# Kernel optimization log

Measured on AMD Instinct MI355X. Metric: run time of the kernel, lower is better.

Reference implementation:

```python
import jax, jax.numpy as jnp
import numpy as np

N = 100000
E = 1600000
NEG_SLOPE = 0.2


def gat_layer(x, W, al, ar, b, src, dst):
    """DGL GATConv (no dropout, no residual, bias=True, activation=None).
    x: [N, in]; W: [in, H*D]; al, ar, b: [H, D]. Returns [N, H, D]."""
    H, D = al.shape
    feat = (x @ W).reshape(N, H, D)               # [N,H,D]
    el = jnp.sum(feat * al, axis=-1)              # [N,H]
    er = jnp.sum(feat * ar, axis=-1)              # [N,H]
    e = jax.nn.leaky_relu(el[src] + er[dst], NEG_SLOPE)  # [E,H]
    # segment softmax over incoming edges of each dst node
    emax = jax.lax.stop_gradient(jax.ops.segment_max(e, dst, num_segments=N))
    ex = jnp.exp(e - emax[dst])                   # [E,H]
    denom = jax.ops.segment_sum(ex, dst, num_segments=N)  # [N,H]
    alpha = ex / jnp.where(denom[dst] == 0, 1.0, denom[dst])  # [E,H]
    msg = feat[src] * alpha[..., None]            # [E,H,D] gather + weight
    out = jax.ops.segment_sum(msg, dst, num_segments=N)    # [N,H,D] scatter-add
    return out + b[None, :, :]


def setup_inputs() -> dict:
    key = jax.random.key(0)
    ks = jax.random.split(key, 12)
    in_size, hid, out_size, heads = 128, 32, 16, 4
    x = jax.random.normal(ks[0], (N, in_size), dtype=jnp.float32)
    src = jax.random.randint(ks[1], (E,), 0, N, dtype=jnp.int32)
    dst = jax.random.randint(ks[2], (E,), 0, N, dtype=jnp.int32)
    W1 = jax.random.normal(ks[3], (in_size, heads * hid), dtype=jnp.float32) * (1.0 / np.sqrt(in_size))
    al1 = jax.random.normal(ks[4], (heads, hid), dtype=jnp.float32) * 0.1
    ar1 = jax.random.normal(ks[5], (heads, hid), dtype=jnp.float32) * 0.1
    b1 = jnp.zeros((heads, hid), dtype=jnp.float32)
    W2 = jax.random.normal(ks[6], (hid, out_size), dtype=jnp.float32) * (1.0 / np.sqrt(hid))
    al2 = jax.random.normal(ks[7], (1, out_size), dtype=jnp.float32) * 0.1
    ar2 = jax.random.normal(ks[8], (1, out_size), dtype=jnp.float32) * 0.1
    b2 = jnp.zeros((1, out_size), dtype=jnp.float32)
    return {"x": x, "src": src, "dst": dst, "W1": W1, "al1": al1, "ar1": ar1,
            "b1": b1, "W2": W2, "al2": al2, "ar2": ar2, "b2": b2}


def reference(x, src, dst, W1, al1, ar1, b1, W2, al2, ar2, b2):
    h = gat_layer(x, W1, al1, ar1, b1, src, dst)   # [N, heads, hid]
    h = jax.nn.relu(jnp.mean(h, axis=1))           # mean over heads + relu
    h = gat_layer(h, W2, al2, ar2, b2, src, dst)   # [N, 1, out]
    return h.reshape(N, -1)                        # flatten
```

## Files before the change

kernel.cpp:

```cpp
#include <hip/hip_runtime.h>
#include <hip/hip_bf16.h>

#define NEG_SLOPE 0.2f
#define LOG2E 1.44269504f
#define G_SHIFT 7
#define GSZ 128
#define CHUNK 4096

typedef __attribute__((ext_vector_type(8))) __bf16 bf16x8;
typedef __attribute__((ext_vector_type(4))) float f32x4;

__device__ __forceinline__ unsigned short f2bf(float f) {
    unsigned u = __float_as_uint(f);
    unsigned r = (u + 0x7fffu + ((u >> 16) & 1u)) >> 16;
    return (unsigned short)r;
}
__device__ __forceinline__ float bflo(unsigned v) { return __uint_as_float(v << 16); }
__device__ __forceinline__ float bfhi(unsigned v) { return __uint_as_float(v & 0xffff0000u); }

__global__ __launch_bounds__(256) void coarse_scatter(
    const int* __restrict__ src, const int* __restrict__ dst,
    int* __restrict__ gcursor, unsigned* __restrict__ inter, int NB, int E) {
    __shared__ int hist[800];
    __shared__ int lbase[800];
    __shared__ int gbase[800];
    __shared__ unsigned stage[CHUNK];
    __shared__ unsigned short bstage[CHUNK];

    const int tid = threadIdx.x;
    const int e0 = blockIdx.x * CHUNK;
    const int cnt = min(CHUNK, E - e0);

    for (int i = tid; i < NB; i += 256) hist[i] = 0;
    __syncthreads();

    unsigned pk[16];
    int bb[16];
#pragma unroll
    for (int r = 0; r < 16; ++r) {
        int idx = tid + r * 256;
        if (idx < cnt) {
            int s = src[e0 + idx];
            int d = dst[e0 + idx];
            pk[r] = ((unsigned)s << G_SHIFT) | (unsigned)(d & (GSZ - 1));
            bb[r] = d >> G_SHIFT;
            atomicAdd(&hist[bb[r]], 1);
        }
    }
    __syncthreads();
    if (tid < 64) {
        int carry = 0;
        for (int i = 0; i < NB; i += 64) {
            int v = (i + tid < NB) ? hist[i + tid] : 0;
            int xv = v;
            for (int o = 1; o < 64; o <<= 1) {
                int tt = __shfl_up(xv, o, 64);
                if (tid >= o) xv += tt;
            }
            if (i + tid < NB) lbase[i + tid] = carry + xv - v;
            carry += __shfl(xv, 63, 64);
        }
    }
    __syncthreads();
    for (int i = tid; i < NB; i += 256) {
        int hh = hist[i];
        gbase[i] = (hh > 0) ? (i * CHUNK + atomicAdd(&gcursor[i], hh)) : 0;
    }
    __syncthreads();
    for (int i = tid; i < NB; i += 256) hist[i] = 0;
    __syncthreads();
#pragma unroll
    for (int r = 0; r < 16; ++r) {
        int idx = tid + r * 256;
        if (idx < cnt) {
            int b = bb[r];
            int rk = atomicAdd(&hist[b], 1);
            int pos = lbase[b] + rk;
            stage[pos] = pk[r];
            bstage[pos] = (unsigned short)b;
        }
    }
    __syncthreads();
#pragma unroll
    for (int r = 0; r < 16; ++r) {
        int idx = tid + r * 256;
        if (idx < cnt) {
            int b = (int)bstage[idx];
            inter[gbase[b] + (idx - lbase[b])] = stage[idx];
        }
    }
}

__global__ __launch_bounds__(256) void fine_scatter(
    const unsigned* __restrict__ inter, const int* __restrict__ gcursor,
    int* __restrict__ deg, int* __restrict__ rowptr, int* __restrict__ esrc,
    int N, int NB) {
    __shared__ int h[GSZ];
    __shared__ int lb[GSZ];
    __shared__ int stage[CHUNK];
    __shared__ int redsum[256];
    const int b = blockIdx.x;
    const int tid = threadIdx.x;
    const int cnt = gcursor[b];
    const unsigned* ep = inter + (size_t)b * CHUNK;

    {
        int s = 0;
        for (int i = tid; i < b; i += 256) s += gcursor[i];
        redsum[tid] = s;
        __syncthreads();
        for (int o = 128; o > 0; o >>= 1) {
            if (tid < o) redsum[tid] += redsum[tid + o];
            __syncthreads();
        }
    }
    const int base = redsum[0];

    if (tid < GSZ) h[tid] = 0;
    __syncthreads();

    int ss[16];
    unsigned char ln[16];
    int nr = 0;
    for (int idx = tid; idx < cnt; idx += 256) {
        unsigned ed = ep[idx];
        ss[nr] = (int)(ed >> G_SHIFT);
        int l = (int)(ed & (GSZ - 1));
        ln[nr++] = (unsigned char)l;
        atomicAdd(&h[l], 1);
    }
    __syncthreads();
    if (tid < 64) {
        int carry = 0;
        for (int i = 0; i < GSZ; i += 64) {
            int v = h[i + tid];
            int xv = v;
            for (int o = 1; o < 64; o <<= 1) {
                int tt = __shfl_up(xv, o, 64);
                if (tid >= o) xv += tt;
            }
            lb[i + tid] = carry + xv - v;
            carry += __shfl(xv, 63, 64);
        }
    }
    __syncthreads();
    if (tid < GSZ) {
        int node = b * GSZ + tid;
        if (node < N) {
            deg[node] = h[tid];
            rowptr[node] = base + lb[tid];
        }
        h[tid] = 0;
    }
    __syncthreads();
    for (int r = 0; r < nr; ++r) {
        int l = ln[r];
        int rk = atomicAdd(&h[l], 1);
        stage[lb[l] + rk] = ss[r];
    }
    __syncthreads();
    for (int idx = tid; idx < cnt; idx += 256) esrc[base + idx] = stage[idx];
}

__global__ __launch_bounds__(128) void wconv_kernel(
    const float* __restrict__ W, unsigned short* __restrict__ wtb) {
    int c = blockIdx.x;
    int k = threadIdx.x;
    wtb[c * 128 + k] = f2bf(W[k * 128 + c]);
}

#define GSTRIDE 136
__global__ __launch_bounds__(256) void gemm1_mfma(
    const float* __restrict__ x, const unsigned short* __restrict__ wtb,
    const float* __restrict__ al, const float* __restrict__ ar,
    unsigned short* __restrict__ featb, float* __restrict__ el,
    float* __restrict__ er, int N) {
    __shared__ unsigned short xs[128][GSTRIDE];
    __shared__ unsigned short ws[128][GSTRIDE];
    const int t = threadIdx.x;
    const int m0 = blockIdx.x * 128;
    const int w = t >> 6;
    const int l = t & 63;
    const int lr = l & 15;
    const int lg = l >> 4;

    {
        const uint4* wv = (const uint4*)wtb;
#pragma unroll
        for (int rr = 0; rr < 8; ++rr) {
            int q = t + 256 * rr;
            int c = q >> 4, kb = q & 15;
            uint4 v = wv[q];
            *((uint4*)&ws[c][kb * 8]) = v;
        }
    }
    {
#pragma unroll
        for (int rr = 0; rr < 16; ++rr) {
            int q = t + 256 * rr;
            int row = q >> 5, c4 = q & 31;
            int gm = m0 + row;
            if (gm >= N) gm = N - 1;
            float4 v = *((const float4*)(x + (size_t)gm * 128 + c4 * 4));
            ushort4 o;
            o.x = f2bf(v.x); o.y = f2bf(v.y); o.z = f2bf(v.z); o.w = f2bf(v.w);
            *((ushort4*)&xs[row][c4 * 4]) = o;
        }
    }
    __syncthreads();

    f32x4 acc[2][8];
#pragma unroll
    for (int i = 0; i < 2; ++i)
#pragma unroll
        for (int j = 0; j < 8; ++j) acc[i][j] = (f32x4){0.f, 0.f, 0.f, 0.f};

#pragma unroll
    for (int kk = 0; kk < 4; ++kk) {
        const int k0 = kk * 32 + lg * 8;
        bf16x8 a0 = *((const bf16x8*)&xs[w * 32 + lr][k0]);
        bf16x8 a1 = *((const bf16x8*)&xs[w * 32 + 16 + lr][k0]);
#pragma unroll
        for (int nj = 0; nj < 8; ++nj) {
            bf16x8 bfr = *((const bf16x8*)&ws[nj * 16 + lr][k0]);
            acc[0][nj] = __builtin_amdgcn_mfma_f32_16x16x32_bf16(a0, bfr, acc[0][nj], 0, 0, 0);
            acc[1][nj] = __builtin_amdgcn_mfma_f32_16x16x32_bf16(a1, bfr, acc[1][nj], 0, 0, 0);
        }
    }
    __syncthreads();
#pragma unroll
    for (int mi = 0; mi < 2; ++mi)
#pragma unroll
        for (int r = 0; r < 4; ++r) {
            int row = w * 32 + mi * 16 + lg * 4 + r;
#pragma unroll
            for (int nj = 0; nj < 8; ++nj)
                xs[row][nj * 16 + lr] = f2bf(acc[mi][nj][r]);
        }
    __syncthreads();
    {
        int row = t >> 1, half = t & 1;
        int gm = m0 + row;
        if (gm < N) {
            float pl0 = 0.f, pl1 = 0.f, pr0 = 0.f, pr1 = 0.f;
            const unsigned short* xr = &xs[row][half * 64];
            uint4* outp = (uint4*)(featb + (size_t)gm * 128 + half * 64);
#pragma unroll
            for (int b8 = 0; b8 < 8; ++b8) {
                uint4 v = *((const uint4*)(xr + b8 * 8));
                int cb = half * 64 + b8 * 8;
                float4 a0 = *((const float4*)(al + cb));
                float4 a1 = *((const float4*)(al + cb + 4));
                float4 r0 = *((const float4*)(ar + cb));
                float4 r1 = *((const float4*)(ar + cb + 4));
                float f0 = bflo(v.x), f1 = bfhi(v.x), f2 = bflo(v.y), f3 = bfhi(v.y);
                float f4 = bflo(v.z), f5 = bfhi(v.z), f6 = bflo(v.w), f7 = bfhi(v.w);
                float sl = f0 * a0.x + f1 * a0.y + f2 * a0.z + f3 * a0.w
                         + f4 * a1.x + f5 * a1.y + f6 * a1.z + f7 * a1.w;
                float sr = f0 * r0.x + f1 * r0.y + f2 * r0.z + f3 * r0.w
                         + f4 * r1.x + f5 * r1.y + f6 * r1.z + f7 * r1.w;
                if (b8 < 4) { pl0 += sl; pr0 += sr; } else { pl1 += sl; pr1 += sr; }
                outp[b8] = v;
            }
            el[gm * 4 + half * 2 + 0] = pl0 * LOG2E;
            el[gm * 4 + half * 2 + 1] = pl1 * LOG2E;
            er[gm * 4 + half * 2 + 0] = pr0 * LOG2E;
            er[gm * 4 + half * 2 + 1] = pr1 * LOG2E;
        }
    }
}

__global__ __launch_bounds__(256) void pull1_kernel(
    const int* __restrict__ rowptr, const int* __restrict__ deg,
    const int* __restrict__ esrc, const float* __restrict__ el,
    const float* __restrict__ er, const unsigned short* __restrict__ featb,
    const float* __restrict__ b,
    const float* __restrict__ W2, const float* __restrict__ al2,
    const float* __restrict__ ar2, float* __restrict__ feat2,
    float* __restrict__ el2, float* __restrict__ er2, int N) {
    int tid = blockIdx.x * 256 + threadIdx.x;
    int node = tid >> 4;
    int lane = threadIdx.x & 15;
    if (node >= N) return;
    int h = lane >> 2;
    int dq = lane & 3;
    int start = rowptr[node];
    int cnt = deg[node];
    float er_nh = er[node * 4 + h];
    const int* ep = esrc + start;
    const unsigned short* fb = featb + h * 32 + dq * 8;

    float acc[8];
#pragma unroll
    for (int j = 0; j < 8; ++j) acc[j] = 0.f;
    float sumex = 0.f;

    int i = 0;
    for (; i + 8 <= cnt; i += 8) {
        int s[8]; float e[8]; uint4 u[8];
#pragma unroll
        for (int j = 0; j < 8; ++j) s[j] = ep[i + j];
#pragma unroll
        for (int j = 0; j < 8; ++j) u[j] = *((const uint4*)(fb + (size_t)s[j] * 128));
#pragma unroll
        for (int j = 0; j < 8; ++j) e[j] = el[s[j] * 4 + h];
#pragma unroll
        for (int j = 0; j < 8; ++j) {
            float v = e[j] + er_nh;
            v = fmaxf(v, NEG_SLOPE * v);
            float xx = exp2f(v);
            sumex += xx;
            acc[0] += xx * bflo(u[j].x); acc[1] += xx * bfhi(u[j].x);
            acc[2] += xx * bflo(u[j].y); acc[3] += xx * bfhi(u[j].y);
            acc[4] += xx * bflo(u[j].z); acc[5] += xx * bfhi(u[j].z);
            acc[6] += xx * bflo(u[j].w); acc[7] += xx * bfhi(u[j].w);
        }
    }
    for (; i + 4 <= cnt; i += 4) {
        int s[4]; float e[4]; uint4 u[4];
#pragma unroll
        for (int j = 0; j < 4; ++j) s[j] = ep[i + j];
#pragma unroll
        for (int j = 0; j < 4; ++j) u[j] = *((const uint4*)(fb + (size_t)s[j] * 128));
#pragma unroll
        for (int j = 0; j < 4; ++j) e[j] = el[s[j] * 4 + h];
#pragma unroll
        for (int j = 0; j < 4; ++j) {
            float v = e[j] + er_nh;
            v = fmaxf(v, NEG_SLOPE * v);
            float xx = exp2f(v);
            sumex += xx;
            acc[0] += xx * bflo(u[j].x); acc[1] += xx * bfhi(u[j].x);
            acc[2] += xx * bflo(u[j].y); acc[3] += xx * bfhi(u[j].y);
            acc[4] += xx * bflo(u[j].z); acc[5] += xx * bfhi(u[j].z);
            acc[6] += xx * bflo(u[j].w); acc[7] += xx * bfhi(u[j].w);
        }
    }
    for (; i < cnt; ++i) {
        int s = ep[i];
        float v = el[s * 4 + h] + er_nh;
        v = fmaxf(v, NEG_SLOPE * v);
        float xx = exp2f(v);
        sumex += xx;
        uint4 u = *((const uint4*)(fb + (size_t)s * 128));
        acc[0] += xx * bflo(u.x); acc[1] += xx * bfhi(u.x);
        acc[2] += xx * bflo(u.y); acc[3] += xx * bfhi(u.y);
        acc[4] += xx * bflo(u.z); acc[5] += xx * bfhi(u.z);
        acc[6] += xx * bflo(u.w); acc[7] += xx * bfhi(u.w);
    }

    float inv = 1.f / ((sumex == 0.f) ? 1.f : sumex);
    float4 bb0 = *((const float4*)(b + h * 32 + dq * 8));
    float4 bb1 = *((const float4*)(b + h * 32 + dq * 8 + 4));
    float o[8];
    o[0] = acc[0] * inv + bb0.x; o[1] = acc[1] * inv + bb0.y;
    o[2] = acc[2] * inv + bb0.z; o[3] = acc[3] * inv + bb0.w;
    o[4] = acc[4] * inv + bb1.x; o[5] = acc[5] * inv + bb1.y;
    o[6] = acc[6] * inv + bb1.z; o[7] = acc[7] * inv + bb1.w;
#pragma unroll
    for (int j = 0; j < 8; ++j) {
        o[j] += __shfl_xor(o[j], 4);
        o[j] += __shfl_xor(o[j], 8);
        o[j] = fmaxf(o[j] * 0.25f, 0.f);
    }
    int c = lane;
    float fc = 0.f;
#pragma unroll
    for (int q = 0; q < 4; ++q) {
#pragma unroll
        for (int j = 0; j < 8; ++j) {
            float hv = __shfl(o[j], q, 16);
            fc += hv * W2[(q * 8 + j) * 16 + c];
        }
    }
    float pl = fc * al2[c];
    float pr = fc * ar2[c];
    pl += __shfl_xor(pl, 1); pl += __shfl_xor(pl, 2);
    pl += __shfl_xor(pl, 4); pl += __shfl_xor(pl, 8);
    pr += __shfl_xor(pr, 1); pr += __shfl_xor(pr, 2);
    pr += __shfl_xor(pr, 4); pr += __shfl_xor(pr, 8);
    feat2[(size_t)node * 16 + c] = fc;
    if (lane == 0) {
        el2[node] = pl * LOG2E;
        er2[node] = pr * LOG2E;
    }
}

__global__ __launch_bounds__(256) void pull2_kernel(
    const int* __restrict__ rowptr, const int* __restrict__ deg,
    const int* __restrict__ esrc, const float* __restrict__ el,
    const float* __restrict__ er, const float* __restrict__ feat,
    const float* __restrict__ b, float* __restrict__ outp, int N) {
    int tid = blockIdx.x * 256 + threadIdx.x;
    int node = tid >> 2;
    int d4 = threadIdx.x & 3;
    if (node >= N) return;

    int start = rowptr[node];
    int cnt = deg[node];
    float er_n = er[node];
    const int* ep = esrc + start;
    const float* fb = feat + d4 * 4;

    float4 acc = make_float4(0.f, 0.f, 0.f, 0.f);
    float sumex = 0.f;
    int i = 0;
    for (; i + 8 <= cnt; i += 8) {
        int s[8];
#pragma unroll
        for (int j = 0; j < 8; ++j) s[j] = ep[i + j];
        float ee[8];
        float4 ff[8];
#pragma unroll
        for (int j = 0; j < 8; ++j) {
            ee[j] = el[s[j]];
            ff[j] = *((const float4*)(fb + (size_t)s[j] * 16));
        }
#pragma unroll
        for (int j = 0; j < 8; ++j) {
            float v = ee[j] + er_n;
            v = fmaxf(v, NEG_SLOPE * v);
            float ex = exp2f(v);
            acc.x += ex * ff[j].x; acc.y += ex * ff[j].y;
            acc.z += ex * ff[j].z; acc.w += ex * ff[j].w;
            sumex += ex;
        }
    }
    for (; i + 4 <= cnt; i += 4) {
        int s[4];
#pragma unroll
        for (int j = 0; j < 4; ++j) s[j] = ep[i + j];
        float ee[4];
        float4 ff[4];
#pragma unroll
        for (int j = 0; j < 4; ++j) {
            ee[j] = el[s[j]];
            ff[j] = *((const float4*)(fb + (size_t)s[j] * 16));
        }
#pragma unroll
        for (int j = 0; j < 4; ++j) {
            float v = ee[j] + er_n;
            v = fmaxf(v, NEG_SLOPE * v);
            float ex = exp2f(v);
            acc.x += ex * ff[j].x; acc.y += ex * ff[j].y;
            acc.z += ex * ff[j].z; acc.w += ex * ff[j].w;
            sumex += ex;
        }
    }
    for (; i < cnt; ++i) {
        int s = ep[i];
        float v = el[s] + er_n;
        v = fmaxf(v, NEG_SLOPE * v);
        float ex = exp2f(v);
        float4 f = *((const float4*)(fb + (size_t)s * 16));
        acc.x += ex * f.x; acc.y += ex * f.y;
        acc.z += ex * f.z; acc.w += ex * f.w;
        sumex += ex;
    }
    float inv = 1.f / ((sumex == 0.f) ? 1.f : sumex);
    float4 bb = *((const float4*)(b + d4 * 4));
    float4 o;
    o.x = acc.x * inv + bb.x;
    o.y = acc.y * inv + bb.y;
    o.z = acc.z * inv + bb.z;
    o.w = acc.w * inv + bb.w;
    *((float4*)(outp + (size_t)node * 16 + d4 * 4)) = o;
}

extern "C" void kernel_launch(void* const* d_in, const int* in_sizes, int n_in,
                              void* d_out, int out_size, void* d_ws, size_t ws_size,
                              hipStream_t stream) {
    const float* x   = (const float*)d_in[0];
    const int*   src = (const int*)d_in[1];
    const int*   dst = (const int*)d_in[2];
    const float* W1  = (const float*)d_in[3];
    const float* al1 = (const float*)d_in[4];
    const float* ar1 = (const float*)d_in[5];
    const float* b1  = (const float*)d_in[6];
    const float* W2  = (const float*)d_in[7];
    const float* al2 = (const float*)d_in[8];
    const float* ar2 = (const float*)d_in[9];
    const float* b2  = (const float*)d_in[10];

    const int E = in_sizes[1];
    const int N = in_sizes[0] / 128;
    const int H1 = 4, C1 = 128;
    const int D2 = 16;
    const int NB = (N + GSZ - 1) / GSZ;
    const int NCH = (E + CHUNK - 1) / CHUNK;

    char* p = (char*)d_ws;
    auto alloc_f = [&](size_t n) { float* q = (float*)p; p += n * sizeof(float); return q; };
    auto alloc_i = [&](size_t n) { int* q = (int*)p; p += n * sizeof(int); return q; };

    unsigned short* feat1b = (unsigned short*)p; p += (size_t)N * C1 * sizeof(unsigned short);
    float* el1   = alloc_f((size_t)N * H1);
    float* er1   = alloc_f((size_t)N * H1);
    float* feat2 = alloc_f((size_t)N * D2);
    float* el2   = alloc_f(N);
    float* er2   = alloc_f(N);
    int* deg     = alloc_i(N);
    int* rowptr  = alloc_i(N);
    int* esrc    = alloc_i(E);
    int* gcursor = alloc_i(NB);
    unsigned* inter = (unsigned*)alloc_i((size_t)NB * CHUNK);
    unsigned short* wtb = (unsigned short*)p; p += (size_t)128 * 128 * sizeof(unsigned short);

    const int TB = 256;
    auto blocks = [&](long long n) { return (int)((n + TB - 1) / TB); };

    hipMemsetAsync(gcursor, 0, (size_t)NB * sizeof(int), stream);
    wconv_kernel<<<128, 128, 0, stream>>>(W1, wtb);
    coarse_scatter<<<NCH, TB, 0, stream>>>(src, dst, gcursor, inter, NB, E);
    fine_scatter<<<NB, TB, 0, stream>>>(inter, gcursor, deg, rowptr, esrc, N, NB);

    gemm1_mfma<<<(N + 127) / 128, TB, 0, stream>>>(x, wtb, al1, ar1, feat1b, el1, er1, N);
    pull1_kernel<<<blocks((long long)N * 16), TB, 0, stream>>>(
        rowptr, deg, esrc, el1, er1, feat1b, b1,
        W2, al2, ar2, feat2, el2, er2, N);

    pull2_kernel<<<blocks((long long)N * 4), TB, 0, stream>>>(
        rowptr, deg, esrc, el2, er2, feat2, b2, (float*)d_out, N);
}
```

Before: 262.2 us.

## Store layer-2 features in bf16, use packed float2 FMAs, shrink pull blocks

The layer-2 feature array written by pull1 and gathered by pull2 is now stored as bf16 instead of fp32, which halves the bytes of that random gather. Both pull kernels accumulate through 2-wide float vectors so the compiler can emit packed FMA instructions. Block size for both pull kernels drops from 256 to 128 threads. The bf16 storage adds rounding error to the second-layer inputs.

```diff
diff --git a/kernel.cpp b/kernel.cpp
--- a/kernel.cpp
+++ b/kernel.cpp
@@ -9,6 +9,7 @@
 
 typedef __attribute__((ext_vector_type(8))) __bf16 bf16x8;
 typedef __attribute__((ext_vector_type(4))) float f32x4;
+typedef __attribute__((ext_vector_type(2))) float f32x2;
 
 __device__ __forceinline__ unsigned short f2bf(float f) {
     unsigned u = __float_as_uint(f);
@@ -17,6 +18,9 @@
 }
 __device__ __forceinline__ float bflo(unsigned v) { return __uint_as_float(v << 16); }
 __device__ __forceinline__ float bfhi(unsigned v) { return __uint_as_float(v & 0xffff0000u); }
+__device__ __forceinline__ float bf2f(unsigned short v) {
+    return __uint_as_float((unsigned)v << 16);
+}
 
 __global__ __launch_bounds__(256) void coarse_scatter(
     const int* __restrict__ src, const int* __restrict__ dst,
@@ -270,15 +274,15 @@
     }
 }
 
-__global__ __launch_bounds__(256) void pull1_kernel(
+__global__ __launch_bounds__(128) void pull1_kernel(
     const int* __restrict__ rowptr, const int* __restrict__ deg,
     const int* __restrict__ esrc, const float* __restrict__ el,
     const float* __restrict__ er, const unsigned short* __restrict__ featb,
     const float* __restrict__ b,
     const float* __restrict__ W2, const float* __restrict__ al2,
-    const float* __restrict__ ar2, float* __restrict__ feat2,
+    const float* __restrict__ ar2, unsigned short* __restrict__ feat2b,
     float* __restrict__ el2, float* __restrict__ er2, int N) {
-    int tid = blockIdx.x * 256 + threadIdx.x;
+    int tid = blockIdx.x * 128 + threadIdx.x;
     int node = tid >> 4;
     int lane = threadIdx.x & 15;
     if (node >= N) return;
@@ -290,9 +294,9 @@
     const int* ep = esrc + start;
     const unsigned short* fb = featb + h * 32 + dq * 8;
 
-    float acc[8];
-#pragma unroll
-    for (int j = 0; j < 8; ++j) acc[j] = 0.f;
+    f32x2 acc2[4];
+#pragma unroll
+    for (int j = 0; j < 4; ++j) acc2[j] = (f32x2){0.f, 0.f};
     float sumex = 0.f;
 
     int i = 0;
@@ -310,10 +314,11 @@
             v = fmaxf(v, NEG_SLOPE * v);
             float xx = exp2f(v);
             sumex += xx;
-            acc[0] += xx * bflo(u[j].x); acc[1] += xx * bfhi(u[j].x);
-            acc[2] += xx * bflo(u[j].y); acc[3] += xx * bfhi(u[j].y);
-            acc[4] += xx * bflo(u[j].z); acc[5] += xx * bfhi(u[j].z);
-            acc[6] += xx * bflo(u[j].w); acc[7] += xx * bfhi(u[j].w);
+            f32x2 xx2 = (f32x2){xx, xx};
+            acc2[0] += xx2 * (f32x2){bflo(u[j].x), bfhi(u[j].x)};
+            acc2[1] += xx2 * (f32x2){bflo(u[j].y), bfhi(u[j].y)};
+            acc2[2] += xx2 * (f32x2){bflo(u[j].z), bfhi(u[j].z)};
+            acc2[3] += xx2 * (f32x2){bflo(u[j].w), bfhi(u[j].w)};
         }
     }
     for (; i + 4 <= cnt; i += 4) {
@@ -330,10 +335,11 @@
             v = fmaxf(v, NEG_SLOPE * v);
             float xx = exp2f(v);
             sumex += xx;
-            acc[0] += xx * bflo(u[j].x); acc[1] += xx * bfhi(u[j].x);
-            acc[2] += xx * bflo(u[j].y); acc[3] += xx * bfhi(u[j].y);
-            acc[4] += xx * bflo(u[j].z); acc[5] += xx * bfhi(u[j].z);
-            acc[6] += xx * bflo(u[j].w); acc[7] += xx * bfhi(u[j].w);
+            f32x2 xx2 = (f32x2){xx, xx};
+            acc2[0] += xx2 * (f32x2){bflo(u[j].x), bfhi(u[j].x)};
+            acc2[1] += xx2 * (f32x2){bflo(u[j].y), bfhi(u[j].y)};
+            acc2[2] += xx2 * (f32x2){bflo(u[j].z), bfhi(u[j].z)};
+            acc2[3] += xx2 * (f32x2){bflo(u[j].w), bfhi(u[j].w)};
         }
     }
     for (; i < cnt; ++i) {
@@ -343,20 +349,21 @@
         float xx = exp2f(v);
         sumex += xx;
         uint4 u = *((const uint4*)(fb + (size_t)s * 128));
-        acc[0] += xx * bflo(u.x); acc[1] += xx * bfhi(u.x);
-        acc[2] += xx * bflo(u.y); acc[3] += xx * bfhi(u.y);
-        acc[4] += xx * bflo(u.z); acc[5] += xx * bfhi(u.z);
-        acc[6] += xx * bflo(u.w); acc[7] += xx * bfhi(u.w);
+        f32x2 xx2 = (f32x2){xx, xx};
+        acc2[0] += xx2 * (f32x2){bflo(u.x), bfhi(u.x)};
+        acc2[1] += xx2 * (f32x2){bflo(u.y), bfhi(u.y)};
+        acc2[2] += xx2 * (f32x2){bflo(u.z), bfhi(u.z)};
+        acc2[3] += xx2 * (f32x2){bflo(u.w), bfhi(u.w)};
     }
 
     float inv = 1.f / ((sumex == 0.f) ? 1.f : sumex);
     float4 bb0 = *((const float4*)(b + h * 32 + dq * 8));
     float4 bb1 = *((const float4*)(b + h * 32 + dq * 8 + 4));
     float o[8];
-    o[0] = acc[0] * inv + bb0.x; o[1] = acc[1] * inv + bb0.y;
-    o[2] = acc[2] * inv + bb0.z; o[3] = acc[3] * inv + bb0.w;
-    o[4] = acc[4] * inv + bb1.x; o[5] = acc[5] * inv + bb1.y;
-    o[6] = acc[6] * inv + bb1.z; o[7] = acc[7] * inv + bb1.w;
+    o[0] = acc2[0].x * inv + bb0.x; o[1] = acc2[0].y * inv + bb0.y;
+    o[2] = acc2[1].x * inv + bb0.z; o[3] = acc2[1].y * inv + bb0.w;
+    o[4] = acc2[2].x * inv + bb1.x; o[5] = acc2[2].y * inv + bb1.y;
+    o[6] = acc2[3].x * inv + bb1.z; o[7] = acc2[3].y * inv + bb1.w;
 #pragma unroll
     for (int j = 0; j < 8; ++j) {
         o[j] += __shfl_xor(o[j], 4);
@@ -379,19 +386,19 @@
     pl += __shfl_xor(pl, 4); pl += __shfl_xor(pl, 8);
     pr += __shfl_xor(pr, 1); pr += __shfl_xor(pr, 2);
     pr += __shfl_xor(pr, 4); pr += __shfl_xor(pr, 8);
-    feat2[(size_t)node * 16 + c] = fc;
+    feat2b[(size_t)node * 16 + c] = f2bf(fc);
     if (lane == 0) {
         el2[node] = pl * LOG2E;
         er2[node] = pr * LOG2E;
     }
 }
 
-__global__ __launch_bounds__(256) void pull2_kernel(
+__global__ __launch_bounds__(128) void pull2_kernel(
     const int* __restrict__ rowptr, const int* __restrict__ deg,
     const int* __restrict__ esrc, const float* __restrict__ el,
-    const float* __restrict__ er, const float* __restrict__ feat,
+    const float* __restrict__ er, const unsigned short* __restrict__ feat2b,
     const float* __restrict__ b, float* __restrict__ outp, int N) {
-    int tid = blockIdx.x * 256 + threadIdx.x;
+    int tid = blockIdx.x * 128 + threadIdx.x;
     int node = tid >> 2;
     int d4 = threadIdx.x & 3;
     if (node >= N) return;
@@ -400,9 +407,10 @@
     int cnt = deg[node];
     float er_n = er[node];
     const int* ep = esrc + start;
-    const float* fb = feat + d4 * 4;
-
-    float4 acc = make_float4(0.f, 0.f, 0.f, 0.f);
+    const unsigned short* fb = feat2b + d4 * 4;
+
+    f32x2 acc01 = (f32x2){0.f, 0.f};
+    f32x2 acc23 = (f32x2){0.f, 0.f};
     float sumex = 0.f;
     int i = 0;
     for (; i + 8 <= cnt; i += 8) {
@@ -410,20 +418,21 @@
 #pragma unroll
         for (int j = 0; j < 8; ++j) s[j] = ep[i + j];
         float ee[8];
-        float4 ff[8];
+        ushort4 ff[8];
 #pragma unroll
         for (int j = 0; j < 8; ++j) {
             ee[j] = el[s[j]];
-            ff[j] = *((const float4*)(fb + (size_t)s[j] * 16));
+            ff[j] = *((const ushort4*)(fb + (size_t)s[j] * 16));
         }
 #pragma unroll
         for (int j = 0; j < 8; ++j) {
             float v = ee[j] + er_n;
             v = fmaxf(v, NEG_SLOPE * v);
             float ex = exp2f(v);
-            acc.x += ex * ff[j].x; acc.y += ex * ff[j].y;
-            acc.z += ex * ff[j].z; acc.w += ex * ff[j].w;
             sumex += ex;
+            f32x2 ex2 = (f32x2){ex, ex};
+            acc01 += ex2 * (f32x2){bf2f(ff[j].x), bf2f(ff[j].y)};
+            acc23 += ex2 * (f32x2){bf2f(ff[j].z), bf2f(ff[j].w)};
         }
     }
     for (; i + 4 <= cnt; i += 4) {
@@ -431,20 +440,21 @@
 #pragma unroll
         for (int j = 0; j < 4; ++j) s[j] = ep[i + j];
         float ee[4];
-        float4 ff[4];
+        ushort4 ff[4];
 #pragma unroll
         for (int j = 0; j < 4; ++j) {
             ee[j] = el[s[j]];
-            ff[j] = *((const float4*)(fb + (size_t)s[j] * 16));
+            ff[j] = *((const ushort4*)(fb + (size_t)s[j] * 16));
         }
 #pragma unroll
         for (int j = 0; j < 4; ++j) {
             float v = ee[j] + er_n;
             v = fmaxf(v, NEG_SLOPE * v);
             float ex = exp2f(v);
-            acc.x += ex * ff[j].x; acc.y += ex * ff[j].y;
-            acc.z += ex * ff[j].z; acc.w += ex * ff[j].w;
             sumex += ex;
+            f32x2 ex2 = (f32x2){ex, ex};
+            acc01 += ex2 * (f32x2){bf2f(ff[j].x), bf2f(ff[j].y)};
+            acc23 += ex2 * (f32x2){bf2f(ff[j].z), bf2f(ff[j].w)};
         }
     }
     for (; i < cnt; ++i) {
@@ -452,18 +462,19 @@
         float v = el[s] + er_n;
         v = fmaxf(v, NEG_SLOPE * v);
         float ex = exp2f(v);
-        float4 f = *((const float4*)(fb + (size_t)s * 16));
-        acc.x += ex * f.x; acc.y += ex * f.y;
-        acc.z += ex * f.z; acc.w += ex * f.w;
         sumex += ex;
+        ushort4 f = *((const ushort4*)(fb + (size_t)s * 16));
+        f32x2 ex2 = (f32x2){ex, ex};
+        acc01 += ex2 * (f32x2){bf2f(f.x), bf2f(f.y)};
+        acc23 += ex2 * (f32x2){bf2f(f.z), bf2f(f.w)};
     }
     float inv = 1.f / ((sumex == 0.f) ? 1.f : sumex);
     float4 bb = *((const float4*)(b + d4 * 4));
     float4 o;
-    o.x = acc.x * inv + bb.x;
-    o.y = acc.y * inv + bb.y;
-    o.z = acc.z * inv + bb.z;
-    o.w = acc.w * inv + bb.w;
+    o.x = acc01.x * inv + bb.x;
+    o.y = acc01.y * inv + bb.y;
+    o.z = acc23.x * inv + bb.z;
+    o.w = acc23.y * inv + bb.w;
     *((float4*)(outp + (size_t)node * 16 + d4 * 4)) = o;
 }
 
@@ -494,9 +505,9 @@
     auto alloc_i = [&](size_t n) { int* q = (int*)p; p += n * sizeof(int); return q; };
 
     unsigned short* feat1b = (unsigned short*)p; p += (size_t)N * C1 * sizeof(unsigned short);
+    unsigned short* feat2b = (unsigned short*)p; p += (size_t)N * D2 * sizeof(unsigned short);
     float* el1   = alloc_f((size_t)N * H1);
     float* er1   = alloc_f((size_t)N * H1);
-    float* feat2 = alloc_f((size_t)N * D2);
     float* el2   = alloc_f(N);
     float* er2   = alloc_f(N);
     int* deg     = alloc_i(N);
@@ -507,7 +518,6 @@
     unsigned short* wtb = (unsigned short*)p; p += (size_t)128 * 128 * sizeof(unsigned short);
 
     const int TB = 256;
-    auto blocks = [&](long long n) { return (int)((n + TB - 1) / TB); };
 
     hipMemsetAsync(gcursor, 0, (size_t)NB * sizeof(int), stream);
     wconv_kernel<<<128, 128, 0, stream>>>(W1, wtb);
@@ -515,10 +525,10 @@
     fine_scatter<<<NB, TB, 0, stream>>>(inter, gcursor, deg, rowptr, esrc, N, NB);
 
     gemm1_mfma<<<(N + 127) / 128, TB, 0, stream>>>(x, wtb, al1, ar1, feat1b, el1, er1, N);
-    pull1_kernel<<<blocks((long long)N * 16), TB, 0, stream>>>(
+    pull1_kernel<<<(int)(((long long)N * 16 + 127) / 128), 128, 0, stream>>>(
         rowptr, deg, esrc, el1, er1, feat1b, b1,
-        W2, al2, ar2, feat2, el2, er2, N);
-
-    pull2_kernel<<<blocks((long long)N * 4), TB, 0, stream>>>(
-        rowptr, deg, esrc, el2, er2, feat2, b2, (float*)d_out, N);
-}
+        W2, al2, ar2, feat2b, el2, er2, N);
+
+    pull2_kernel<<<(int)(((long long)N * 4 + 127) / 128), 128, 0, stream>>>(
+        rowptr, deg, esrc, el2, er2, feat2b, b2, (float*)d_out, N);
+}
```

New measurement: 261.4 us. No clear change (-0.3%).
